# Kernel optimization log

Hardware: AMD Instinct MI355X
Metric: run time of the kernel (lower is better)

Reference implementation:

```python
import jax, jax.numpy as jnp
import numpy as np

N_NODES = 50000
N_EDGES = 800000
HID = 128


def setup_inputs() -> dict:
    key = jax.random.key(0)
    ks = jax.random.split(key, 8)
    h = jax.random.normal(ks[0], (N_NODES, HID), dtype=jnp.float32)
    edge_index = jax.random.randint(ks[1], (2, N_EDGES), 0, N_NODES, dtype=jnp.int64)
    edge_attr = jax.random.normal(ks[2], (N_EDGES, HID), dtype=jnp.float32)
    # MLP params: Linear(3H -> H), Linear(H -> 1). Stored as [in, out] so y = x @ W + b.
    s1 = 1.0 / np.sqrt(3 * HID)
    W1 = jax.random.uniform(ks[3], (3 * HID, HID), minval=-s1, maxval=s1, dtype=jnp.float32)
    b1 = jax.random.uniform(ks[4], (HID,), minval=-s1, maxval=s1, dtype=jnp.float32)
    s2 = 1.0 / np.sqrt(HID)
    W2 = jax.random.uniform(ks[5], (HID, 1), minval=-s2, maxval=s2, dtype=jnp.float32)
    b2 = jax.random.uniform(ks[6], (1,), minval=-s2, maxval=s2, dtype=jnp.float32)
    return {"h": h, "edge_index": edge_index, "edge_attr": edge_attr,
            "W1": W1, "b1": b1, "W2": W2, "b2": b2}


def reference(h, edge_index, edge_attr, W1, b1, W2, b2):
    row, col = edge_index[0], edge_index[1]
    h_i = h[row]                      # [E, H] gather of source nodes
    h_j = h[col]                      # [E, H] gather of target nodes
    # Split first Linear over the concat [h_i, h_j, edge_attr] to avoid a [E, 3H] buffer.
    Wa, Wb, Wc = W1[:HID], W1[HID:2 * HID], W1[2 * HID:]
    pre = h_i @ Wa + h_j @ Wb + edge_attr @ Wc + b1      # [E, H]
    a = jax.nn.elu(pre) @ W2 + b2                        # [E, 1]
    a = jax.nn.leaky_relu(a, negative_slope=0.2)
    alpha = jax.nn.softmax(a, axis=0)                    # softmax over all edges (dim=0)
    h_agg = jnp.zeros_like(h).at[row].add(alpha * h_j)   # scatter-add weighted neighbors
    return h_agg
```

## Files before the change

### kernel.cpp

```cpp
#include <hip/hip_runtime.h>
#include <hip/hip_bf16.h>
#include <math.h>

#define NNODES 50000
#define NEDGES 800000
#define HID    128
#define NB_SCAN 196
#define NB_EDGE 6250

typedef short bf16x8 __attribute__((ext_vector_type(8)));
typedef float f32x4  __attribute__((ext_vector_type(4)));

__device__ __forceinline__ unsigned short bf16_rn(float x) {
    union { float f; unsigned int u; } v; v.f = x;
    unsigned int r = v.u + 0x7fffu + ((v.u >> 16) & 1u);
    return (unsigned short)(r >> 16);
}
__device__ __forceinline__ float bf16_to_f(unsigned short u) {
    union { unsigned int u; float f; } v; v.u = ((unsigned int)u) << 16;
    return v.f;
}

__device__ __forceinline__ float expm1_fast(float x) {
    float t = 1.9841270e-4f;
    t = fmaf(t, x, 1.3888889e-3f);
    t = fmaf(t, x, 8.3333333e-3f);
    t = fmaf(t, x, 4.1666668e-2f);
    t = fmaf(t, x, 0.16666667f);
    t = fmaf(t, x, 0.5f);
    t = fmaf(t, x, 1.0f);
    float poly = x * t;
    float ex   = __expf(x) - 1.0f;
    return (x > -0.25f) ? poly : ex;
}

__global__ void k_prep(const float* __restrict__ W1, unsigned short* __restrict__ Wt)
{
    const float* Wc = W1 + 256 * 128;
    int base = (blockIdx.x * 256 + threadIdx.x) * 4;
#pragma unroll
    for (int i = 0; i < 4; ++i) {
        int idx = base + i;
        int c = idx >> 7, k = idx & 127;
        Wt[c * 128 + k] = bf16_rn(Wc[k * 128 + c]);
    }
}

__global__ __launch_bounds__(256) void k_gemm_node(
    const float* __restrict__ h, const float* __restrict__ W1,
    const float* __restrict__ b1, unsigned short* __restrict__ Hab)
{
    __shared__ float at[32][132];
    __shared__ float bt[32][128];

    const int tid = threadIdx.x;
    const int tx  = tid & 15;
    const int ty  = tid >> 4;
    const int nb  = blockIdx.x * 128;
    const int by  = blockIdx.y;
    const float* W = W1 + by * 128 * 128;

    float acc[8][8];
#pragma unroll
    for (int j = 0; j < 8; ++j)
#pragma unroll
        for (int c = 0; c < 8; ++c) acc[j][c] = 0.0f;

    for (int ks = 0; ks < 128; ks += 32) {
#pragma unroll
        for (int p = 0; p < 16; ++p) {
            int i  = (tid >> 5) + p * 8;
            int kk = tid & 31;
            int n  = nb + i;
            at[kk][i] = (n < NNODES) ? h[n * 128 + ks + kk] : 0.0f;
        }
#pragma unroll
        for (int p = 0; p < 16; ++p) {
            int kk = (tid >> 7) + p * 2;
            int c  = tid & 127;
            bt[kk][c] = W[(ks + kk) * 128 + c];
        }
        __syncthreads();
#pragma unroll
        for (int k = 0; k < 32; ++k) {
            float av[8], bv[8];
            *(float4*)&av[0] = *(const float4*)&at[k][ty * 8];
            *(float4*)&av[4] = *(const float4*)&at[k][ty * 8 + 4];
            *(float4*)&bv[0] = *(const float4*)&bt[k][tx * 8];
            *(float4*)&bv[4] = *(const float4*)&bt[k][tx * 8 + 4];
#pragma unroll
            for (int j = 0; j < 8; ++j)
#pragma unroll
                for (int c = 0; c < 8; ++c)
                    acc[j][c] = fmaf(av[j], bv[c], acc[j][c]);
        }
        __syncthreads();
    }

    float b1v[8];
    if (by == 0) {
        *(float4*)&b1v[0] = *(const float4*)&b1[tx * 8];
        *(float4*)&b1v[4] = *(const float4*)&b1[tx * 8 + 4];
    } else {
#pragma unroll
        for (int c = 0; c < 8; ++c) b1v[c] = 0.0f;
    }
#pragma unroll
    for (int j = 0; j < 8; ++j) {
        int n = nb + ty * 8 + j;
        if (n < NNODES) {
            unsigned short o[8];
#pragma unroll
            for (int c = 0; c < 8; ++c) o[c] = bf16_rn(acc[j][c] + b1v[c]);
            unsigned short* dst = Hab + (size_t)n * 256 + by * 128 + tx * 8;
            *(int4*)dst = *(int4*)&o[0];
        }
    }
}

__global__ __launch_bounds__(256) void k_edge_mfma(
    const float* __restrict__ ea, const int* __restrict__ eidx,
    const unsigned short* __restrict__ Wt, const float* __restrict__ W2,
    const float* __restrict__ b2, const unsigned short* __restrict__ Hab,
    float* __restrict__ a_out, int* __restrict__ hist,
    float* __restrict__ bmax, float* __restrict__ bsumE)
{
    const int tid  = threadIdx.x;
    const int w    = tid >> 6;
    const int l    = tid & 63;
    const int quad = l >> 4;
    const int lm   = l & 15;
    const int wm   = w * 32;
    const int ebase = blockIdx.x * 128;

    __shared__ __align__(16) unsigned short wlds[16384];
    __shared__ float sred[8];

#pragma unroll
    for (int i = 0; i < 8; ++i) {
        int idx16 = i * 2048 + tid * 8;
        int c = idx16 >> 7;
        bf16x8 v = *(const bf16x8*)(Wt + idx16);
        int byte = (idx16 * 2) ^ (((c >> 3) & 15) << 4);
        *(bf16x8*)((char*)wlds + byte) = v;
    }

    f32x4 acc[2][8] = {};

    int rows0[4], cols0[4], rows1[4], cols1[4];
    {
        const int e40 = ebase + wm + quad * 4;
        const int e41 = e40 + 16;
        int4 r0 = *(const int4*)(eidx + e40);
        int4 c0 = *(const int4*)(eidx + NEDGES + e40);
        int4 r1 = *(const int4*)(eidx + e41);
        int4 c1 = *(const int4*)(eidx + NEDGES + e41);
        rows0[0] = r0.x; rows0[1] = r0.y; rows0[2] = r0.z; rows0[3] = r0.w;
        cols0[0] = c0.x; cols0[1] = c0.y; cols0[2] = c0.z; cols0[3] = c0.w;
        rows1[0] = r1.x; rows1[1] = r1.y; rows1[2] = r1.z; rows1[3] = r1.w;
        cols1[0] = c1.x; cols1[1] = c1.y; cols1[2] = c1.z; cols1[3] = c1.w;
    }
    if (lm == 0) {
#pragma unroll
        for (int r = 0; r < 4; ++r) {
            atomicAdd(&hist[rows0[r]], 1);
            atomicAdd(&hist[rows1[r]], 1);
        }
    }

    const float* abase0 = ea + (size_t)(ebase + wm + lm) * 128 + quad * 8;
    const float* abase1 = abase0 + 16 * 128;
    float4 raw[2][2][2];
    raw[0][0][0] = *(const float4*)(abase0);
    raw[0][0][1] = *(const float4*)(abase0 + 4);
    raw[0][1][0] = *(const float4*)(abase1);
    raw[0][1][1] = *(const float4*)(abase1 + 4);

    bf16x8 hav[2][4], hbv[2][4];

    __syncthreads();

#pragma unroll
    for (int stage = 0; stage < 4; ++stage) {
        const int ks  = stage * 32;
        const int cur = stage & 1, nxt = cur ^ 1;
        if (stage < 3) {
            const int ko = ks + 32;
            raw[nxt][0][0] = *(const float4*)(abase0 + ko);
            raw[nxt][0][1] = *(const float4*)(abase0 + ko + 4);
            raw[nxt][1][0] = *(const float4*)(abase1 + ko);
            raw[nxt][1][1] = *(const float4*)(abase1 + ko + 4);
        }
        if (stage == 3) {
#pragma unroll
            for (int r = 0; r < 4; ++r) {
                hav[0][r] = *(const bf16x8*)(Hab + (size_t)rows0[r] * 256 + lm * 8);
                hbv[0][r] = *(const bf16x8*)(Hab + (size_t)cols0[r] * 256 + 128 + lm * 8);
                hav[1][r] = *(const bf16x8*)(Hab + (size_t)rows1[r] * 256 + lm * 8);
                hbv[1][r] = *(const bf16x8*)(Hab + (size_t)cols1[r] * 256 + 128 + lm * 8);
            }
        }
        bf16x8 bfrag[8];
#pragma unroll
        for (int nt = 0; nt < 8; ++nt) {
            const int c = lm * 8 + nt;
            const int byte = (c * 256 + (ks + quad * 8) * 2) ^ ((lm & 15) << 4);
            bfrag[nt] = *(const bf16x8*)((const char*)wlds + byte);
        }
        bf16x8 afrag[2];
#pragma unroll
        for (int mt = 0; mt < 2; ++mt) {
            float4 x0 = raw[cur][mt][0];
            float4 x1 = raw[cur][mt][1];
            bf16x8 f;
            f[0] = (short)bf16_rn(x0.x); f[1] = (short)bf16_rn(x0.y);
            f[2] = (short)bf16_rn(x0.z); f[3] = (short)bf16_rn(x0.w);
            f[4] = (short)bf16_rn(x1.x); f[5] = (short)bf16_rn(x1.y);
            f[6] = (short)bf16_rn(x1.z); f[7] = (short)bf16_rn(x1.w);
            afrag[mt] = f;
        }
#pragma unroll
        for (int mt = 0; mt < 2; ++mt)
#pragma unroll
            for (int nt = 0; nt < 8; ++nt)
                acc[mt][nt] = __builtin_amdgcn_mfma_f32_16x16x32_bf16(
                    afrag[mt], bfrag[nt], acc[mt][nt], 0, 0, 0);
    }

    float w2v[8];
    *(float4*)&w2v[0] = *(const float4*)&W2[lm * 8];
    *(float4*)&w2v[4] = *(const float4*)&W2[lm * 8 + 4];
    const float b2s = b2[0];

    float avl[2] = { -INFINITY, -INFINITY };

#pragma unroll
    for (int mt = 0; mt < 2; ++mt) {
        const int e4 = ebase + wm + mt * 16 + quad * 4;

        float s0 = 0.f, s1 = 0.f, s2 = 0.f, s3 = 0.f;
#pragma unroll
        for (int r = 0; r < 4; ++r) {
            float sr = 0.f;
#pragma unroll
            for (int nt = 0; nt < 8; ++nt) {
                float ha  = bf16_to_f((unsigned short)hav[mt][r][nt]);
                float hb  = bf16_to_f((unsigned short)hbv[mt][r][nt]);
                float pre = acc[mt][nt][r] + ha + hb;
                float el  = pre > 0.f ? pre : expm1_fast(pre);
                sr = fmaf(el, w2v[nt], sr);
            }
            if (r == 0) s0 = sr; else if (r == 1) s1 = sr; else if (r == 2) s2 = sr; else s3 = sr;
        }
#pragma unroll
        for (int m = 1; m < 16; m <<= 1) {
            s0 += __shfl_xor(s0, m, 64);
            s1 += __shfl_xor(s1, m, 64);
            s2 += __shfl_xor(s2, m, 64);
            s3 += __shfl_xor(s3, m, 64);
        }
        if (lm < 4) {
            float sum = (lm == 0) ? s0 : (lm == 1) ? s1 : (lm == 2) ? s2 : s3;
            sum += b2s;
            float av = sum >= 0.f ? sum : 0.2f * sum;
            a_out[e4 + lm] = av;
            avl[mt] = av;
        }
    }

    float m = fmaxf(avl[0], avl[1]);
#pragma unroll
    for (int msk = 1; msk < 64; msk <<= 1) m = fmaxf(m, __shfl_xor(m, msk, 64));
    if (l == 0) sred[w] = m;
    __syncthreads();
    float mb = fmaxf(fmaxf(sred[0], sred[1]), fmaxf(sred[2], sred[3]));
    float es = 0.f;
    if (avl[0] > -INFINITY)
        es = expf(avl[0] - mb) + expf(avl[1] - mb);
#pragma unroll
    for (int msk = 1; msk < 64; msk <<= 1) es += __shfl_xor(es, msk, 64);
    if (l == 0) sred[4 + w] = es;
    __syncthreads();
    if (tid == 0) {
        bmax[blockIdx.x]  = mb;
        bsumE[blockIdx.x] = sred[4] + sred[5] + sred[6] + sred[7];
    }
}

__global__ void k_scan_blk(const int* __restrict__ hist, int* __restrict__ offsets,
                           int* __restrict__ bsum)
{
    __shared__ int sd[256];
    int t = threadIdx.x, i = blockIdx.x * 256 + t;
    int v = (i < NNODES) ? hist[i] : 0;
    sd[t] = v; __syncthreads();
    for (int off = 1; off < 256; off <<= 1) {
        int add = (t >= off) ? sd[t - off] : 0;
        __syncthreads();
        sd[t] += add;
        __syncthreads();
    }
    if (i < NNODES) offsets[i] = sd[t] - v;
    if (t == 255) bsum[blockIdx.x] = sd[255];
}

__global__ void k_scan_top(const int* __restrict__ bsum, int* __restrict__ bpre,
                           int* __restrict__ offsets)
{
    __shared__ int sd[256];
    int t = threadIdx.x;
    int v = (t < NB_SCAN) ? bsum[t] : 0;
    sd[t] = v; __syncthreads();
    for (int off = 1; off < 256; off <<= 1) {
        int add = (t >= off) ? sd[t - off] : 0;
        __syncthreads();
        sd[t] += add;
        __syncthreads();
    }
    if (t < NB_SCAN) bpre[t] = sd[t] - v;
    if (t == 255) offsets[NNODES] = sd[255];
}

__global__ void k_scan_add(int* __restrict__ offsets, const int* __restrict__ bpre)
{
    int i = blockIdx.x * 256 + threadIdx.x;
    if (i < NNODES) offsets[i] += bpre[i >> 8];
}

__global__ __launch_bounds__(1024) void k_final(
    const float* __restrict__ bmax, const float* __restrict__ bsumE,
    float* __restrict__ mz)
{
    __shared__ float sd[1024];
    int tid = threadIdx.x;
    float m = -INFINITY;
    for (int i = tid; i < NB_EDGE; i += 1024) m = fmaxf(m, bmax[i]);
    sd[tid] = m; __syncthreads();
    for (int off = 512; off > 0; off >>= 1) {
        if (tid < off) sd[tid] = fmaxf(sd[tid], sd[tid + off]);
        __syncthreads();
    }
    float M = sd[0];
    __syncthreads();
    float s = 0.f;
    for (int i = tid; i < NB_EDGE; i += 1024) s += bsumE[i] * expf(bmax[i] - M);
    sd[tid] = s; __syncthreads();
    for (int off = 512; off > 0; off >>= 1) {
        if (tid < off) sd[tid] += sd[tid + off];
        __syncthreads();
    }
    if (tid == 0) { mz[0] = M; mz[1] = 1.0f / sd[0]; }
}

__global__ void k_scatter(const int* __restrict__ eidx, const int* __restrict__ offsets,
                          int* __restrict__ cursor, const float* __restrict__ a,
                          const float* __restrict__ mz, int2* __restrict__ pairs)
{
    int e = blockIdx.x * 256 + threadIdx.x;
    if (e < NEDGES) {
        int r    = eidx[e];
        float al = expf(a[e] - mz[0]) * mz[1];
        int pos  = offsets[r] + atomicAdd(&cursor[r], 1);
        pairs[pos] = make_int2(__float_as_int(al), eidx[NEDGES + e]);
    }
}

__global__ __launch_bounds__(256) void k_agg(
    const float* __restrict__ h, const int2* __restrict__ pairs,
    const int* __restrict__ offsets, float* __restrict__ out)
{
    int node = blockIdx.x * 4 + (threadIdx.x >> 6);
    int lane = threadIdx.x & 63;
    if (node >= NNODES) return;
    int s0 = offsets[node], s1 = offsets[node + 1];
    float2 acc = make_float2(0.0f, 0.0f);
    int i = s0;
    for (; i + 8 <= s1; i += 8) {
        int2 p[8];
#pragma unroll
        for (int r = 0; r < 8; ++r) p[r] = pairs[i + r];
        float2 hv[8];
#pragma unroll
        for (int r = 0; r < 8; ++r)
            hv[r] = *(const float2*)(h + (size_t)p[r].y * 128 + lane * 2);
#pragma unroll
        for (int r = 0; r < 8; ++r) {
            float al = __int_as_float(p[r].x);
            acc.x = fmaf(al, hv[r].x, acc.x);
            acc.y = fmaf(al, hv[r].y, acc.y);
        }
    }
    for (; i < s1; ++i) {
        int2 p = pairs[i];
        float al = __int_as_float(p.x);
        float2 hj = *(const float2*)(h + (size_t)p.y * 128 + lane * 2);
        acc.x = fmaf(al, hj.x, acc.x);
        acc.y = fmaf(al, hj.y, acc.y);
    }
    *(float2*)(out + (size_t)node * 128 + lane * 2) = acc;
}

extern "C" void kernel_launch(void* const* d_in, const int* in_sizes, int n_in,
                              void* d_out, int out_size, void* d_ws, size_t ws_size,
                              hipStream_t stream)
{
    const float* h    = (const float*)d_in[0];
    const int*   eidx = (const int*)d_in[1];
    const float* ea   = (const float*)d_in[2];
    const float* W1   = (const float*)d_in[3];
    const float* b1   = (const float*)d_in[4];
    const float* W2   = (const float*)d_in[5];
    const float* b2   = (const float*)d_in[6];
    float* out = (float*)d_out;

    char* ws = (char*)d_ws;
    unsigned short* Hab = (unsigned short*)(ws);
    float* a_arr   = (float*)(ws + 25600000);
    int2*  pairs   = (int2*) (ws + 28800000);
    int*   offsets = (int*)  (ws + 35200000);
    int*   cursor  = (int*)  (ws + 35400192);
    float* bmax    = (float*)(ws + 35600384);
    float* bsumE   = (float*)(ws + 35625984);
    float* mz      = (float*)(ws + 35651584);
    unsigned short* Wt = (unsigned short*)(ws + 35651648);
    int*   bsum_s  = (int*)  (ws + 35684416);
    int*   bpre_s  = (int*)  (ws + 35685440);

    hipMemsetAsync(cursor, 0, NNODES * sizeof(int), stream);

    k_prep<<<16, 256, 0, stream>>>(W1, Wt);
    k_gemm_node<<<dim3((NNODES + 127) / 128, 2), 256, 0, stream>>>(h, W1, b1, Hab);

    k_edge_mfma<<<NB_EDGE, 256, 0, stream>>>(ea, eidx, Wt, W2, b2, Hab,
                                             a_arr, cursor, bmax, bsumE);

    k_scan_blk<<<NB_SCAN, 256, 0, stream>>>(cursor, offsets, bsum_s);
    k_scan_top<<<1, 256, 0, stream>>>(bsum_s, bpre_s, offsets);
    k_scan_add<<<NB_SCAN, 256, 0, stream>>>(offsets, bpre_s);
    hipMemsetAsync(cursor, 0, NNODES * sizeof(int), stream);

    k_final<<<1, 1024, 0, stream>>>(bmax, bsumE, mz);
    k_scatter<<<(NEDGES + 255) / 256, 256, 0, stream>>>(eidx, offsets, cursor,
                                                        a_arr, mz, pairs);
    k_agg<<<(NNODES + 3) / 4, 256, 0, stream>>>(h, pairs, offsets, out);
}
```

Baseline: 803.5 us.

## Use split-bf16 MFMA for node GEMM, hoist gathers, merge cursor memsets

After: 807.4 us. About the same (+0.5%).

```diff
diff --git a/kernel.cpp b/kernel.cpp
--- a/kernel.cpp
+++ b/kernel.cpp
@@ -34,86 +34,124 @@
     return (x > -0.25f) ? poly : ex;
 }
 
-__global__ void k_prep(const float* __restrict__ W1, unsigned short* __restrict__ Wt)
-{
+__global__ void k_prep(const float* __restrict__ W1, unsigned short* __restrict__ Wt,
+                       unsigned short* __restrict__ WH, unsigned short* __restrict__ WL)
+{
+    int t = blockIdx.x * 256 + threadIdx.x;
     const float* Wc = W1 + 256 * 128;
-    int base = (blockIdx.x * 256 + threadIdx.x) * 4;
-#pragma unroll
-    for (int i = 0; i < 4; ++i) {
-        int idx = base + i;
-        int c = idx >> 7, k = idx & 127;
+#pragma unroll
+    for (int i = t * 4; i < t * 4 + 4; ++i) {
+        int c = i >> 7, k = i & 127;
         Wt[c * 128 + k] = bf16_rn(Wc[k * 128 + c]);
     }
-}
-
-__global__ __launch_bounds__(256) void k_gemm_node(
-    const float* __restrict__ h, const float* __restrict__ W1,
-    const float* __restrict__ b1, unsigned short* __restrict__ Hab)
-{
-    __shared__ float at[32][132];
-    __shared__ float bt[32][128];
-
-    const int tid = threadIdx.x;
-    const int tx  = tid & 15;
-    const int ty  = tid >> 4;
-    const int nb  = blockIdx.x * 128;
-    const int by  = blockIdx.y;
-    const float* W = W1 + by * 128 * 128;
-
-    float acc[8][8];
-#pragma unroll
-    for (int j = 0; j < 8; ++j)
-#pragma unroll
-        for (int c = 0; c < 8; ++c) acc[j][c] = 0.0f;
-
-    for (int ks = 0; ks < 128; ks += 32) {
-#pragma unroll
-        for (int p = 0; p < 16; ++p) {
-            int i  = (tid >> 5) + p * 8;
-            int kk = tid & 31;
-            int n  = nb + i;
-            at[kk][i] = (n < NNODES) ? h[n * 128 + ks + kk] : 0.0f;
-        }
-#pragma unroll
-        for (int p = 0; p < 16; ++p) {
-            int kk = (tid >> 7) + p * 2;
-            int c  = tid & 127;
-            bt[kk][c] = W[(ks + kk) * 128 + c];
-        }
-        __syncthreads();
-#pragma unroll
-        for (int k = 0; k < 32; ++k) {
-            float av[8], bv[8];
-            *(float4*)&av[0] = *(const float4*)&at[k][ty * 8];
-            *(float4*)&av[4] = *(const float4*)&at[k][ty * 8 + 4];
-            *(float4*)&bv[0] = *(const float4*)&bt[k][tx * 8];
-            *(float4*)&bv[4] = *(const float4*)&bt[k][tx * 8 + 4];
-#pragma unroll
-            for (int j = 0; j < 8; ++j)
-#pragma unroll
-                for (int c = 0; c < 8; ++c)
-                    acc[j][c] = fmaf(av[j], bv[c], acc[j][c]);
-        }
-        __syncthreads();
+#pragma unroll
+    for (int i = t * 8; i < t * 8 + 8; ++i) {
+        int half = i >> 14, c = (i >> 7) & 127, k = i & 127;
+        float v = W1[(half * 128 + k) * 128 + c];
+        unsigned short hi = bf16_rn(v);
+        float res = v - bf16_to_f(hi);
+        WH[i] = hi;
+        WL[i] = bf16_rn(res);
+    }
+}
+
+__global__ __launch_bounds__(256) void k_gemm_mfma(
+    const float* __restrict__ h, const unsigned short* __restrict__ WH,
+    const unsigned short* __restrict__ WL, const float* __restrict__ b1,
+    unsigned short* __restrict__ Hab)
+{
+    const int tid  = threadIdx.x;
+    const int w    = tid >> 6;
+    const int l    = tid & 63;
+    const int quad = l >> 4;
+    const int lm   = l & 15;
+    const int wm   = w * 32;
+    const int nb   = blockIdx.x * 128;
+    const int by   = blockIdx.y;
+    const unsigned short* __restrict__ BH = WH + by * 16384;
+    const unsigned short* __restrict__ BL = WL + by * 16384;
+
+    const int node0 = nb + wm + lm;
+    const int node1 = node0 + 16;
+    const bool v0 = node0 < NNODES, v1 = node1 < NNODES;
+    const float* a0 = h + (size_t)node0 * 128 + quad * 8;
+    const float* a1 = h + (size_t)node1 * 128 + quad * 8;
+    const float4 fz = make_float4(0.f, 0.f, 0.f, 0.f);
+
+    f32x4 acc[2][8] = {};
+    float4 raw[2][2][2];
+    raw[0][0][0] = v0 ? *(const float4*)(a0)     : fz;
+    raw[0][0][1] = v0 ? *(const float4*)(a0 + 4) : fz;
+    raw[0][1][0] = v1 ? *(const float4*)(a1)     : fz;
+    raw[0][1][1] = v1 ? *(const float4*)(a1 + 4) : fz;
+
+#pragma unroll
+    for (int stage = 0; stage < 4; ++stage) {
+        const int ks  = stage * 32;
+        const int cur = stage & 1, nxt = cur ^ 1;
+        if (stage < 3) {
+            const int ko = ks + 32;
+            raw[nxt][0][0] = v0 ? *(const float4*)(a0 + ko)     : fz;
+            raw[nxt][0][1] = v0 ? *(const float4*)(a0 + ko + 4) : fz;
+            raw[nxt][1][0] = v1 ? *(const float4*)(a1 + ko)     : fz;
+            raw[nxt][1][1] = v1 ? *(const float4*)(a1 + ko + 4) : fz;
+        }
+        bf16x8 bh[8], bl[8];
+#pragma unroll
+        for (int nt = 0; nt < 8; ++nt) {
+            const int c = lm * 8 + nt;
+            bh[nt] = *(const bf16x8*)(BH + c * 128 + ks + quad * 8);
+            bl[nt] = *(const bf16x8*)(BL + c * 128 + ks + quad * 8);
+        }
+        bf16x8 ahh[2], ahl[2];
+#pragma unroll
+        for (int mt = 0; mt < 2; ++mt) {
+            float x[8];
+            *(float4*)&x[0] = raw[cur][mt][0];
+            *(float4*)&x[4] = raw[cur][mt][1];
+            bf16x8 fh, fl;
+#pragma unroll
+            for (int j = 0; j < 8; ++j) {
+                unsigned short hi = bf16_rn(x[j]);
+                float res = x[j] - bf16_to_f(hi);
+                fh[j] = (short)hi;
+                fl[j] = (short)bf16_rn(res);
+            }
+            ahh[mt] = fh; ahl[mt] = fl;
+        }
+#pragma unroll
+        for (int mt = 0; mt < 2; ++mt)
+#pragma unroll
+            for (int nt = 0; nt < 8; ++nt) {
+                acc[mt][nt] = __builtin_amdgcn_mfma_f32_16x16x32_bf16(
+                    ahh[mt], bh[nt], acc[mt][nt], 0, 0, 0);
+                acc[mt][nt] = __builtin_amdgcn_mfma_f32_16x16x32_bf16(
+                    ahh[mt], bl[nt], acc[mt][nt], 0, 0, 0);
+                acc[mt][nt] = __builtin_amdgcn_mfma_f32_16x16x32_bf16(
+                    ahl[mt], bh[nt], acc[mt][nt], 0, 0, 0);
+            }
     }
 
     float b1v[8];
     if (by == 0) {
-        *(float4*)&b1v[0] = *(const float4*)&b1[tx * 8];
-        *(float4*)&b1v[4] = *(const float4*)&b1[tx * 8 + 4];
+        *(float4*)&b1v[0] = *(const float4*)&b1[lm * 8];
+        *(float4*)&b1v[4] = *(const float4*)&b1[lm * 8 + 4];
     } else {
 #pragma unroll
-        for (int c = 0; c < 8; ++c) b1v[c] = 0.0f;
-    }
-#pragma unroll
-    for (int j = 0; j < 8; ++j) {
-        int n = nb + ty * 8 + j;
-        if (n < NNODES) {
-            unsigned short o[8];
-#pragma unroll
-            for (int c = 0; c < 8; ++c) o[c] = bf16_rn(acc[j][c] + b1v[c]);
-            unsigned short* dst = Hab + (size_t)n * 256 + by * 128 + tx * 8;
-            *(int4*)dst = *(int4*)&o[0];
+        for (int c = 0; c < 8; ++c) b1v[c] = 0.f;
+    }
+#pragma unroll
+    for (int mt = 0; mt < 2; ++mt) {
+#pragma unroll
+        for (int r = 0; r < 4; ++r) {
+            int node = nb + wm + mt * 16 + quad * 4 + r;
+            if (node < NNODES) {
+                unsigned short o[8];
+#pragma unroll
+                for (int nt = 0; nt < 8; ++nt)
+                    o[nt] = bf16_rn(acc[mt][nt][r] + b1v[nt]);
+                *(int4*)(Hab + (size_t)node * 256 + by * 128 + lm * 8) = *(int4*)&o[0];
+            }
         }
     }
 }
@@ -144,28 +182,19 @@
         int byte = (idx16 * 2) ^ (((c >> 3) & 15) << 4);
         *(bf16x8*)((char*)wlds + byte) = v;
     }
-
-    f32x4 acc[2][8] = {};
+    __syncthreads();
 
     int rows0[4], cols0[4], rows1[4], cols1[4];
+    const int e40 = ebase + wm + quad * 4;
     {
-        const int e40 = ebase + wm + quad * 4;
-        const int e41 = e40 + 16;
         int4 r0 = *(const int4*)(eidx + e40);
         int4 c0 = *(const int4*)(eidx + NEDGES + e40);
-        int4 r1 = *(const int4*)(eidx + e41);
-        int4 c1 = *(const int4*)(eidx + NEDGES + e41);
+        int4 r1 = *(const int4*)(eidx + e40 + 16);
+        int4 c1 = *(const int4*)(eidx + NEDGES + e40 + 16);
         rows0[0] = r0.x; rows0[1] = r0.y; rows0[2] = r0.z; rows0[3] = r0.w;
         cols0[0] = c0.x; cols0[1] = c0.y; cols0[2] = c0.z; cols0[3] = c0.w;
         rows1[0] = r1.x; rows1[1] = r1.y; rows1[2] = r1.z; rows1[3] = r1.w;
         cols1[0] = c1.x; cols1[1] = c1.y; cols1[2] = c1.z; cols1[3] = c1.w;
-    }
-    if (lm == 0) {
-#pragma unroll
-        for (int r = 0; r < 4; ++r) {
-            atomicAdd(&hist[rows0[r]], 1);
-            atomicAdd(&hist[rows1[r]], 1);
-        }
     }
 
     const float* abase0 = ea + (size_t)(ebase + wm + lm) * 128 + quad * 8;
@@ -177,8 +206,16 @@
     raw[0][1][1] = *(const float4*)(abase1 + 4);
 
     bf16x8 hav[2][4], hbv[2][4];
-
-    __syncthreads();
+#pragma unroll
+    for (int r = 0; r < 4; ++r) {
+        hav[0][r] = *(const bf16x8*)(Hab + (size_t)rows0[r] * 256 + lm * 8);
+        hbv[0][r] = *(const bf16x8*)(Hab + (size_t)cols0[r] * 256 + 128 + lm * 8);
+        hav[1][r] = *(const bf16x8*)(Hab + (size_t)rows1[r] * 256 + lm * 8);
+        hbv[1][r] = *(const bf16x8*)(Hab + (size_t)cols1[r] * 256 + 128 + lm * 8);
+    }
+    asm volatile("" ::: "memory");
+
+    f32x4 acc[2][8] = {};
 
 #pragma unroll
     for (int stage = 0; stage < 4; ++stage) {
@@ -191,15 +228,6 @@
             raw[nxt][1][0] = *(const float4*)(abase1 + ko);
             raw[nxt][1][1] = *(const float4*)(abase1 + ko + 4);
         }
-        if (stage == 3) {
-#pragma unroll
-            for (int r = 0; r < 4; ++r) {
-                hav[0][r] = *(const bf16x8*)(Hab + (size_t)rows0[r] * 256 + lm * 8);
-                hbv[0][r] = *(const bf16x8*)(Hab + (size_t)cols0[r] * 256 + 128 + lm * 8);
-                hav[1][r] = *(const bf16x8*)(Hab + (size_t)rows1[r] * 256 + lm * 8);
-                hbv[1][r] = *(const bf16x8*)(Hab + (size_t)cols1[r] * 256 + 128 + lm * 8);
-            }
-        }
         bf16x8 bfrag[8];
 #pragma unroll
         for (int nt = 0; nt < 8; ++nt) {
@@ -285,6 +313,14 @@
         bmax[blockIdx.x]  = mb;
         bsumE[blockIdx.x] = sred[4] + sred[5] + sred[6] + sred[7];
     }
+
+    if (lm == 0) {
+#pragma unroll
+        for (int r = 0; r < 4; ++r) {
+            atomicAdd(&hist[rows0[r]], 1);
+            atomicAdd(&hist[rows1[r]], 1);
+        }
+    }
 }
 
 __global__ void k_scan_blk(const int* __restrict__ hist, int* __restrict__ offsets,
@@ -418,29 +454,31 @@
     float* a_arr   = (float*)(ws + 25600000);
     int2*  pairs   = (int2*) (ws + 28800000);
     int*   offsets = (int*)  (ws + 35200000);
-    int*   cursor  = (int*)  (ws + 35400192);
     float* bmax    = (float*)(ws + 35600384);
     float* bsumE   = (float*)(ws + 35625984);
     float* mz      = (float*)(ws + 35651584);
     unsigned short* Wt = (unsigned short*)(ws + 35651648);
     int*   bsum_s  = (int*)  (ws + 35684416);
     int*   bpre_s  = (int*)  (ws + 35685440);
-
-    hipMemsetAsync(cursor, 0, NNODES * sizeof(int), stream);
-
-    k_prep<<<16, 256, 0, stream>>>(W1, Wt);
-    k_gemm_node<<<dim3((NNODES + 127) / 128, 2), 256, 0, stream>>>(h, W1, b1, Hab);
+    int*   cursorA = (int*)  (ws + 35686464);
+    int*   cursorB = (int*)  (ws + 35886464);
+    unsigned short* WH = (unsigned short*)(ws + 36086464);
+    unsigned short* WL = (unsigned short*)(ws + 36152000);
+
+    hipMemsetAsync(cursorA, 0, 400000, stream);
+
+    k_prep<<<16, 256, 0, stream>>>(W1, Wt, WH, WL);
+    k_gemm_mfma<<<dim3((NNODES + 127) / 128, 2), 256, 0, stream>>>(h, WH, WL, b1, Hab);
 
     k_edge_mfma<<<NB_EDGE, 256, 0, stream>>>(ea, eidx, Wt, W2, b2, Hab,
-                                             a_arr, cursor, bmax, bsumE);
-
-    k_scan_blk<<<NB_SCAN, 256, 0, stream>>>(cursor, offsets, bsum_s);
+                                             a_arr, cursorA, bmax, bsumE);
+
+    k_scan_blk<<<NB_SCAN, 256, 0, stream>>>(cursorA, offsets, bsum_s);
     k_scan_top<<<1, 256, 0, stream>>>(bsum_s, bpre_s, offsets);
     k_scan_add<<<NB_SCAN, 256, 0, stream>>>(offsets, bpre_s);
-    hipMemsetAsync(cursor, 0, NNODES * sizeof(int), stream);
 
     k_final<<<1, 1024, 0, stream>>>(bmax, bsumE, mz);
-    k_scatter<<<(NEDGES + 255) / 256, 256, 0, stream>>>(eidx, offsets, cursor,
+    k_scatter<<<(NEDGES + 255) / 256, 256, 0, stream>>>(eidx, offsets, cursorB,
                                                         a_arr, mz, pairs);
     k_agg<<<(NNODES + 3) / 4, 256, 0, stream>>>(h, pairs, offsets, out);
 }
```
